# Kernel tuning notes

Hardware: AMD Instinct MI355X
Metric: run time of the kernel (lower is better)

## Reference

```python
import jax, jax.numpy as jnp
import numpy as np

BLKQ = 64
BLKK = 64
TOPK_RATIO = 0.125


def setup_inputs() -> dict:
    key = jax.random.key(0)
    ks = jax.random.split(key, 4)
    B, L, H, D = 1, 4096, 16, 64
    q = jax.random.normal(ks[0], (B, L, H, D), jnp.float32)
    k = jax.random.normal(ks[1], (B, L, H, D), jnp.float32)
    v = jax.random.normal(ks[2], (B, L, H, D), jnp.float32)
    w_proj = jax.random.normal(ks[3], (D, D), jnp.float32) * 0.02
    b_proj = jnp.zeros((D,), jnp.float32)
    return {"q": q, "k": k, "v": v, "w_proj": w_proj, "b_proj": b_proj}


def _sparse_linear_attn(q, k, v, w_proj, b_proj):
    # q,k,v: (B, L, H, D) -> (B, H, L, D)
    q = jnp.transpose(q, (0, 2, 1, 3))
    k = jnp.transpose(k, (0, 2, 1, 3))
    v = jnp.transpose(v, (0, 2, 1, 3))
    B, H, L, D = q.shape
    M, N = L // BLKQ, L // BLKK  # L chosen divisible by block sizes (no padding)
    T = max(1, int(TOPK_RATIO * N))  # selected key blocks per query block

    qb = q.reshape(B, H, M, BLKQ, D)
    kb = k.reshape(B, H, N, BLKK, D)
    vb = v.reshape(B, H, N, BLKK, D)

    # --- block map: mean-pooled block descriptors, topk key blocks per query block ---
    qm = qb.mean(axis=3)  # (B,H,M,D)
    km = kb.mean(axis=3)  # (B,H,N,D)
    blk_scores = jnp.einsum('bhmd,bhnd->bhmn', qm, km)
    _, lut = jax.lax.top_k(blk_scores, T)  # (B,H,M,T) int32

    # --- gather selected K/V blocks ---
    b_idx = jnp.arange(B)[:, None, None, None]
    h_idx = jnp.arange(H)[None, :, None, None]
    k_sel = kb[b_idx, h_idx, lut]  # (B,H,M,T,BLKK,D)
    v_sel = vb[b_idx, h_idx, lut]  # (B,H,M,T,BLKK,D)

    # --- block-sparse softmax attention over gathered keys only ---
    scale = D ** (-0.5)
    att = jnp.einsum('bhmqd,bhmtkd->bhmqtk', qb, k_sel) * scale
    att = att.reshape(B, H, M, BLKQ, T * BLKK)
    p = jax.nn.softmax(att, axis=-1)
    o_s = jnp.einsum('bhmqn,bhmnd->bhmqd', p, v_sel.reshape(B, H, M, T * BLKK, D))
    o_s = o_s.reshape(B, H, L, D)

    # --- global linear attention with softmax feature map ---
    q_fm = jax.nn.softmax(q, axis=-1)
    k_fm = jax.nn.softmax(k, axis=-1)
    kvsum = jnp.einsum('bhld,bhle->bhde', k_fm, v)  # (B,H,D,D)
    ksum = k_fm.sum(axis=2)  # (B,H,D)
    num = jnp.einsum('bhld,bhde->bhle', q_fm, kvsum)
    den = jnp.einsum('bhld,bhd->bhl', q_fm, ksum)[..., None] + 1e-6
    o_l = num / den
    o_l = jnp.einsum('bhld,ed->bhle', o_l, w_proj) + b_proj  # nn.Linear: x @ W.T + b

    o = o_s + o_l
    return jnp.transpose(o, (0, 2, 1, 3))  # (B, L, H, D)


def reference(q, k, v, w_proj, b_proj):
    return _sparse_linear_attn(q, k, v, w_proj, b_proj)
```

## Files before the change

### kernel.cpp

```cpp
#include <hip/hip_runtime.h>


#define NH   16
#define DH   64
#define NBLK 64
#define TSEL 8

typedef unsigned short u16;
typedef unsigned int   u32;
typedef __attribute__((ext_vector_type(8))) short short8;
typedef __attribute__((ext_vector_type(4))) float f4;

#define MFMA_BF16(a, b, c) __builtin_amdgcn_mfma_f32_16x16x32_bf16(a, b, c, 0, 0, 0)

__device__ __forceinline__ u16 f2bf_rne(float f) {
  u32 u = __float_as_uint(f);
  u += 0x7fffu + ((u >> 16) & 1u);
  return (u16)(u >> 16);
}
__device__ __forceinline__ u32 pk2(float a, float b) {
  return (u32)f2bf_rne(a) | ((u32)f2bf_rne(b) << 16);
}
__device__ __forceinline__ float bf2f(u16 u) { return __uint_as_float(((u32)u) << 16); }

__device__ __forceinline__ short8 frag_row(const u16* t, int row, int jblk) {
  return *(const short8*)((const char*)t + row * 128 + ((jblk ^ (row & 7)) * 16));
}

__global__ __launch_bounds__(256) void prep_kernel(const float* __restrict__ q,
                                                   const float* __restrict__ k,
                                                   const float* __restrict__ v,
                                                   u16* __restrict__ kT,
                                                   u16* __restrict__ vT,
                                                   float* __restrict__ kvsum,
                                                   float* __restrict__ ksum,
                                                   float* __restrict__ kmv,
                                                   float* __restrict__ qkp2) {
  __shared__ __align__(16) char vsl[8192];
  __shared__ __align__(16) char kfm[8192];
  __shared__ float kcol[64 * 65];
  __shared__ float redmx[256];
  __shared__ float redsm[256];
  __shared__ float kmred[256];
  __shared__ float ksred[256];
  int b = blockIdx.x;
  int n = (b >> 3) & 63;
  int h = 2 * (b & 7) + (b >> 9);
  int tid = threadIdx.x;
  int w = tid >> 6, lane = tid & 63;
  int row = lane, qd = w;
  int lq = lane & 15, quad = lane >> 4;

  float kv[16];
  {
    const float* kr = k + (size_t)(n * 64 + row) * 1024 + h * 64 + qd * 16;
#pragma unroll
    for (int c4 = 0; c4 < 4; c4++) {
      float4 a = *(const float4*)(kr + c4 * 4);
      kv[c4 * 4] = a.x; kv[c4 * 4 + 1] = a.y; kv[c4 * 4 + 2] = a.z; kv[c4 * 4 + 3] = a.w;
    }
  }
  {
    char* ktb = (char*)(kT + ((size_t)(h * 64 + n)) * 4096);
    uint4 w0 = make_uint4(pk2(kv[0], kv[1]), pk2(kv[2], kv[3]),
                          pk2(kv[4], kv[5]), pk2(kv[6], kv[7]));
    uint4 w1 = make_uint4(pk2(kv[8], kv[9]), pk2(kv[10], kv[11]),
                          pk2(kv[12], kv[13]), pk2(kv[14], kv[15]));
    *(uint4*)(ktb + row * 128 + (((2 * qd) ^ (row & 7)) * 16)) = w0;
    *(uint4*)(ktb + row * 128 + (((2 * qd + 1) ^ (row & 7)) * 16)) = w1;
  }
  {
#pragma unroll
    for (int j = 0; j < 16; j++) kcol[(qd * 16 + j) * 65 + row] = kv[j];
  }
  {
    const float* vr = v + (size_t)(n * 64 + row) * 1024 + h * 64 + qd * 16;
    int kb = row >> 3, klo = row & 7;
#pragma unroll
    for (int c4 = 0; c4 < 4; c4++) {
      float4 a = *(const float4*)(vr + c4 * 4);
      float vv[4] = {a.x, a.y, a.z, a.w};
#pragma unroll
      for (int jj = 0; jj < 4; jj++) {
        int e = qd * 16 + c4 * 4 + jj;
        *(u16*)(vsl + e * 128 + ((kb ^ (e & 7)) * 16) + klo * 2) = f2bf_rne(vv[jj]);
      }
    }
  }
  {
    float mx = kv[0];
#pragma unroll
    for (int j = 1; j < 16; j++) mx = fmaxf(mx, kv[j]);
    redmx[qd * 64 + row] = mx;
  }
  __syncthreads();
  {
    int c = tid & 63, g = tid >> 6;
    float pk = 0.f;
#pragma unroll
    for (int i = 0; i < 16; i++) pk += kcol[c * 65 + g * 16 + i];
    kmred[g * 64 + c] = pk;
  }
  {
    float mx = fmaxf(fmaxf(redmx[row], redmx[64 + row]),
                     fmaxf(redmx[128 + row], redmx[192 + row]));
    float sm = 0.f;
#pragma unroll
    for (int j = 0; j < 16; j++) { kv[j] = __expf(kv[j] - mx); sm += kv[j]; }
    redsm[qd * 64 + row] = sm;
  }
  __syncthreads();
  if (tid < 64)
    kmv[h * 4096 + n * 64 + tid] =
        (kmred[tid] + kmred[64 + tid] + kmred[128 + tid] + kmred[192 + tid]) * (1.0f / 64.0f);
  {
    float sm = redsm[row] + redsm[64 + row] + redsm[128 + row] + redsm[192 + row];
    float inv = 1.0f / sm;
    int rb = row >> 3, rlo = row & 7;
#pragma unroll
    for (int j = 0; j < 16; j++) {
      int d = qd * 16 + j;
      *(u16*)(kfm + d * 128 + (((rb) ^ (d & 7)) * 16) + rlo * 2) = f2bf_rne(kv[j] * inv);
    }
  }
  __syncthreads();

  {
    uint4* vt_out = (uint4*)(vT + ((size_t)(h * 64 + n)) * 4096);
    vt_out[tid] = ((const uint4*)vsl)[tid];
    vt_out[256 + tid] = ((const uint4*)vsl)[256 + tid];
  }
  {
    float ks = 0.f;
    short8 x0 = frag_row((const u16*)kfm, lane, 2 * w);
    short8 x1 = frag_row((const u16*)kfm, lane, 2 * w + 1);
#pragma unroll
    for (int e = 0; e < 8; e++) ks += bf2f((u16)x0[e]) + bf2f((u16)x1[e]);
    ksred[tid] = ks;
  }
  {
    f4 acc[4];
    f4 zz = {0.f, 0.f, 0.f, 0.f};
#pragma unroll
    for (int et = 0; et < 4; et++) acc[et] = zz;
#pragma unroll
    for (int ks2 = 0; ks2 < 2; ks2++) {
      short8 a_ = frag_row((const u16*)kfm, w * 16 + lq, 4 * ks2 + quad);
#pragma unroll
      for (int et = 0; et < 4; et++)
        acc[et] = MFMA_BF16(a_, frag_row((const u16*)vsl, et * 16 + lq, 4 * ks2 + quad), acc[et]);
    }
#pragma unroll
    for (int et = 0; et < 4; et++)
#pragma unroll
      for (int r = 0; r < 4; r++)
        atomicAdd(&kvsum[h * 4096 + (w * 16 + quad * 4 + r) * 64 + et * 16 + lq],
                  acc[et][r]);
  }
  __syncthreads();
  if (tid < 64)
    atomicAdd(&ksum[h * 64 + tid], ksred[tid] + ksred[64 + tid] +
                                   ksred[128 + tid] + ksred[192 + tid]);

  {
    const float* base = q + ((size_t)(n * 64 + h * 4)) * 1024 + tid * 4;
    float4 acc = {0.f, 0.f, 0.f, 0.f};
#pragma unroll
    for (int i = 0; i < 4; i++) {
      float4 a = *(const float4*)(base + (size_t)i * 1024);
      acc.x += a.x; acc.y += a.y; acc.z += a.z; acc.w += a.w;
    }
    *(float4*)(qkp2 + ((size_t)(h * 64 + n)) * 1024 + tid * 4) = acc;
  }
}

__global__ __launch_bounds__(256) void post_kernel(const float* __restrict__ qkp2,
                                                   const float* __restrict__ kmv,
                                                   const float* __restrict__ kvsum,
                                                   const float* __restrict__ wgt,
                                                   int* __restrict__ lut,
                                                   u16* __restrict__ m2t) {
  __shared__ float kv_s[64 * 65];
  __shared__ __align__(16) float wt[64 * 20];
  __shared__ __align__(16) float qr_s[4][80];
  int bx = blockIdx.x, tid = threadIdx.x;
  if (bx < 256) {
    int h = bx >> 4, w = tid >> 6, n = tid & 63;
    int m = (bx & 15) * 4 + w;
    float qsum = 0.f;
#pragma unroll
    for (int jg = 0; jg < 16; jg++)
      qsum += qkp2[((size_t)(jg * 64 + m)) * 1024 + h * 64 + n];
    qr_s[w][n] = qsum;
    __syncthreads();
    const float* kr = kmv + h * 4096 + n * 64;
    float s = 0.f;
#pragma unroll
    for (int d = 0; d < 64; d += 4) {
      float4 a = *(const float4*)(kr + d);
      float4 bb = *(const float4*)(&qr_s[w][d]);
      s += a.x * bb.x + a.y * bb.y + a.z * bb.z + a.w * bb.w;
    }
    float my = s;
    for (int t = 0; t < TSEL; t++) {
      float vv = my; int idx = n;
#pragma unroll
      for (int off = 1; off < 64; off <<= 1) {
        float ov = __shfl_xor(vv, off);
        int oi = __shfl_xor(idx, off);
        if (ov > vv || (ov == vv && oi < idx)) { vv = ov; idx = oi; }
      }
      if (n == 0) lut[(h * NBLK + m) * TSEL + t] = idx;
      if (n == idx) my = -INFINITY;
    }
  } else {
    int ib = bx - 256, h = ib >> 2, eq = ib & 3;
#pragma unroll
    for (int jj = 0; jj < 16; jj++) {
      int id2 = jj * 256 + tid;
      kv_s[(id2 >> 6) * 65 + (id2 & 63)] = kvsum[h * 4096 + id2];
    }
#pragma unroll
    for (int i = 0; i < 4; i++) {
      int f = i * 256 + tid;
      wt[(f & 63) * 20 + (f >> 6)] = wgt[(eq * 16 + (f >> 6)) * 64 + (f & 63)];
    }
    __syncthreads();
    int d = tid & 63, g = tid >> 6;
    float4 acc = {0.f, 0.f, 0.f, 0.f};
    for (int jj = 0; jj < 64; jj++) {
      float kvj = kv_s[d * 65 + jj];
      float4 wv = *(const float4*)(&wt[jj * 20 + g * 4]);
      acc.x = fmaf(kvj, wv.x, acc.x);
      acc.y = fmaf(kvj, wv.y, acc.y);
      acc.z = fmaf(kvj, wv.z, acc.z);
      acc.w = fmaf(kvj, wv.w, acc.w);
    }
    char* base = (char*)m2t + (size_t)h * 8192;
    float av[4] = {acc.x, acc.y, acc.z, acc.w};
#pragma unroll
    for (int c = 0; c < 4; c++) {
      int ee = eq * 16 + g * 4 + c;
      *(u16*)(base + ee * 128 + (((d >> 3) ^ (ee & 7)) * 16) + (d & 7) * 2) = f2bf_rne(av[c]);
    }
  }
}

__global__ __launch_bounds__(256, 5) void fused_attn_kernel(const float* __restrict__ q,
                                                            const u16* __restrict__ kT,
                                                            const u16* __restrict__ vT,
                                                            const int* __restrict__ lut,
                                                            const u16* __restrict__ m2t,
                                                            const float* __restrict__ ksum,
                                                            const float* __restrict__ bproj,
                                                            float* __restrict__ out) {
  __shared__ __align__(16) char smem[32768];
  int b = blockIdx.x;
  int m = (b >> 3) & 63;
  int h = 2 * (b & 7) + (b >> 9);
  int tid = threadIdx.x, w = tid >> 6, lane = tid & 63;
  int lq = lane & 15, quad = lane >> 4;
  u16* q_l = (u16*)smem;
  char* buf = smem + 8192;
  char* p_b = smem + 24576 + w * 2048;

  const int lb = (h * NBLK + m) * TSEL;
  int blks[8];
#pragma unroll
  for (int t = 0; t < 8; t++) blks[t] = lut[lb + t];

  {
#pragma unroll
    for (int c = 0; c < 2; c++) {
      int lo = c * 4096 + tid * 16;
      int r = lo >> 7;
      int j = ((lo >> 4) & 7) ^ (r & 7);
      const float* gp = q + ((size_t)(m * 64 + r)) * 1024 + h * 64 + j * 8;
      float4 a = *(const float4*)gp;
      float4 bb = *(const float4*)(gp + 4);
      *(uint4*)(smem + lo) = make_uint4(pk2(a.x, a.y), pk2(a.z, a.w),
                                        pk2(bb.x, bb.y), pk2(bb.z, bb.w));
    }
  }
  {
    const uint4* kt0 = (const uint4*)(kT + ((size_t)(h * 64 + blks[0])) * 4096);
    const uint4* vt0 = (const uint4*)(vT + ((size_t)(h * 64 + blks[0])) * 4096);
    ((uint4*)buf)[tid] = kt0[tid];
    ((uint4*)buf)[256 + tid] = kt0[256 + tid];
    ((uint4*)(buf + 8192))[tid] = vt0[tid];
    ((uint4*)(buf + 8192))[256 + tid] = vt0[256 + tid];
  }
  __syncthreads();

  const int qrow = w * 16 + lq;
  short8 qf[2];
#pragma unroll
  for (int ks = 0; ks < 2; ks++) qf[ks] = frag_row(q_l, qrow, 4 * ks + quad);

  float mrun = -INFINITY, lrun = 0.f;
  f4 o[4];
  f4 zz = {0.f, 0.f, 0.f, 0.f};
#pragma unroll
  for (int et = 0; et < 4; et++) o[et] = zz;

  const u16* kc = (const u16*)buf;
  const u16* vc = (const u16*)(buf + 8192);

  for (int t = 0; t < 8; t++) {
    uint4 pk0, pk1, pv0, pv1;
    if (t < 7) {
      const uint4* ktn = (const uint4*)(kT + ((size_t)(h * 64 + blks[t + 1])) * 4096);
      const uint4* vtn = (const uint4*)(vT + ((size_t)(h * 64 + blks[t + 1])) * 4096);
      pk0 = ktn[tid]; pk1 = ktn[256 + tid];
      pv0 = vtn[tid]; pv1 = vtn[256 + tid];
    }

    f4 s[4];
#pragma unroll
    for (int kt = 0; kt < 4; kt++) s[kt] = zz;
    __builtin_amdgcn_s_setprio(1);
#pragma unroll
    for (int ks = 0; ks < 2; ks++)
#pragma unroll
      for (int kt = 0; kt < 4; kt++)
        s[kt] = MFMA_BF16(frag_row(kc, kt * 16 + lq, 4 * ks + quad), qf[ks], s[kt]);
    __builtin_amdgcn_s_setprio(0);

    float mp = -INFINITY;
#pragma unroll
    for (int kt = 0; kt < 4; kt++)
#pragma unroll
      for (int r = 0; r < 4; r++) mp = fmaxf(mp, s[kt][r]);
    mp = fmaxf(mp, __shfl_xor(mp, 16));
    mp = fmaxf(mp, __shfl_xor(mp, 32));
    mp *= 0.125f;
    if (__any(mp > mrun)) {
      float mn = fmaxf(mrun, mp);
      float al = __expf(mrun - mn);
      mrun = mn;
      lrun *= al;
#pragma unroll
      for (int et = 0; et < 4; et++)
#pragma unroll
        for (int r = 0; r < 4; r++) o[et][r] *= al;
    }
    float rs_ = 0.f;
#pragma unroll
    for (int kt = 0; kt < 4; kt++) {
      float p0 = __expf(fmaf(s[kt][0], 0.125f, -mrun));
      float p1 = __expf(fmaf(s[kt][1], 0.125f, -mrun));
      float p2 = __expf(fmaf(s[kt][2], 0.125f, -mrun));
      float p3 = __expf(fmaf(s[kt][3], 0.125f, -mrun));
      rs_ += p0 + p1 + p2 + p3;
      u32 lo32 = (__float_as_uint(p0) >> 16) | (__float_as_uint(p1) & 0xffff0000u);
      u32 hi32 = (__float_as_uint(p2) >> 16) | (__float_as_uint(p3) & 0xffff0000u);
      int addr = lq * 128 + (((kt * 2 + (quad >> 1)) ^ (lq & 7)) * 16) + (quad & 1) * 8;
      *(uint2*)(p_b + addr) = make_uint2(lo32, hi32);
    }
    rs_ += __shfl_xor(rs_, 16);
    rs_ += __shfl_xor(rs_, 32);
    lrun += rs_;

    __builtin_amdgcn_s_setprio(1);
#pragma unroll
    for (int ks = 0; ks < 2; ks++) {
      short8 pf = frag_row((const u16*)p_b, lq, 4 * ks + quad);
#pragma unroll
      for (int et = 0; et < 4; et++)
        o[et] = MFMA_BF16(frag_row(vc, et * 16 + lq, 4 * ks + quad), pf, o[et]);
    }
    __builtin_amdgcn_s_setprio(0);

    if (t < 7) {
      __syncthreads();
      ((uint4*)buf)[tid] = pk0;
      ((uint4*)buf)[256 + tid] = pk1;
      ((uint4*)(buf + 8192))[tid] = pv0;
      ((uint4*)(buf + 8192))[256 + tid] = pv1;
      __syncthreads();
    }
  }

  __syncthreads();
  {
    const uint4* src = (const uint4*)((const char*)m2t + (size_t)h * 8192);
    ((uint4*)buf)[tid] = src[tid];
    ((uint4*)buf)[256 + tid] = src[256 + tid];
    if (tid < 64) {
      ((float*)(buf + 8192))[tid] = ksum[h * 64 + tid];
      ((float*)(buf + 8448))[tid] = bproj[tid];
    }
  }
  __syncthreads();
  u16* m2_l = (u16*)buf;
  float* ks_s = (float*)(buf + 8192);
  float* b_s = (float*)(buf + 8448);

  short8 qa = frag_row(q_l, qrow, 2 * quad);
  short8 qb = frag_row(q_l, qrow, 2 * quad + 1);
  float ev[16];
  float mx = -INFINITY;
#pragma unroll
  for (int j = 0; j < 8; j++) { float x = bf2f((u16)qa[j]); ev[j] = x; mx = fmaxf(mx, x); }
#pragma unroll
  for (int j = 0; j < 8; j++) { float x = bf2f((u16)qb[j]); ev[8 + j] = x; mx = fmaxf(mx, x); }
  mx = fmaxf(mx, __shfl_xor(mx, 16));
  mx = fmaxf(mx, __shfl_xor(mx, 32));
  float sum = 0.f, eks = 0.f;
#pragma unroll
  for (int j = 0; j < 16; j++) {
    float e = __expf(ev[j] - mx);
    ev[j] = e;
    sum += e;
    eks += e * ks_s[quad * 16 + j];
  }
  sum += __shfl_xor(sum, 16); sum += __shfl_xor(sum, 32);
  eks += __shfl_xor(eks, 16); eks += __shfl_xor(eks, 32);
  float invs = 1.0f / sum;
  float den = fmaf(eks, invs, 1e-6f);
  float scale = invs / den;
  uint4 e0v = make_uint4(pk2(ev[0], ev[1]), pk2(ev[2], ev[3]),
                         pk2(ev[4], ev[5]), pk2(ev[6], ev[7]));
  uint4 e1v = make_uint4(pk2(ev[8], ev[9]), pk2(ev[10], ev[11]),
                         pk2(ev[12], ev[13]), pk2(ev[14], ev[15]));
  *(uint4*)(p_b + lq * 128 + (((2 * quad) ^ (lq & 7)) * 16)) = e0v;
  *(uint4*)(p_b + lq * 128 + (((2 * quad + 1) ^ (lq & 7)) * 16)) = e1v;

  f4 oc[4];
  f4 zz2 = {0.f, 0.f, 0.f, 0.f};
#pragma unroll
  for (int et = 0; et < 4; et++) oc[et] = zz2;
  __builtin_amdgcn_s_setprio(1);
#pragma unroll
  for (int ks2 = 0; ks2 < 2; ks2++) {
    short8 ef = frag_row((const u16*)p_b, lq, 4 * ks2 + quad);
#pragma unroll
    for (int et = 0; et < 4; et++)
      oc[et] = MFMA_BF16(frag_row(m2_l, et * 16 + lq, 4 * ks2 + quad), ef, oc[et]);
  }
  __builtin_amdgcn_s_setprio(0);

  float invl = 1.0f / lrun;
  float* gp = out + ((size_t)(m * 64 + qrow)) * 1024 + h * 64 + quad * 4;
#pragma unroll
  for (int et = 0; et < 4; et++) {
    int e0 = et * 16 + quad * 4;
    float4 ov;
    ov.x = o[et][0] * invl + oc[et][0] * scale + b_s[e0 + 0];
    ov.y = o[et][1] * invl + oc[et][1] * scale + b_s[e0 + 1];
    ov.z = o[et][2] * invl + oc[et][2] * scale + b_s[e0 + 2];
    ov.w = o[et][3] * invl + oc[et][3] * scale + b_s[e0 + 3];
    *(float4*)(gp + et * 16) = ov;
  }
}

extern "C" void kernel_launch(void* const* d_in, const int* in_sizes, int n_in,
                              void* d_out, int out_size, void* d_ws, size_t ws_size,
                              hipStream_t stream) {
  const float* q = (const float*)d_in[0];
  const float* k = (const float*)d_in[1];
  const float* v = (const float*)d_in[2];
  const float* w = (const float*)d_in[3];
  const float* b = (const float*)d_in[4];
  float* out = (float*)d_out;

  u16* kT = (u16*)d_ws;
  u16* vT = kT + 4194304;
  float* qkp2 = (float*)(vT + 4194304);
  float* kmv = qkp2 + 1048576;
  int* lut = (int*)(kmv + 65536);
  float* kvsum = (float*)(lut + 8192);
  float* ksum = kvsum + 65536;
  u16* m2t = (u16*)(ksum + 1024);

  hipMemsetAsync(kvsum, 0, (65536 + 1024) * sizeof(float), stream);
  prep_kernel<<<1024, 256, 0, stream>>>(q, k, v, kT, vT, kvsum, ksum, kmv, qkp2);
  post_kernel<<<320, 256, 0, stream>>>(qkp2, kmv, kvsum, w, lut, m2t);
  fused_attn_kernel<<<1024, 256, 0, stream>>>(q, kT, vT, lut, m2t, ksum, b, out);
}
```

Baseline: 146.7 us.

## Move block top-k into attention kernel and replace atomics with partial-sum reduction

The per-query-block mean pooling and top-k block selection move from post_kernel into fused_attn_kernel, so the lut and qkp2 round trips through global memory go away. The kvsum and ksum atomics in prep_kernel become per-key-block partial writes, and post_kernel reduces them deterministically, which also removes the memset. Q fragments are now loaded directly from global memory instead of being staged through LDS. The smaller LDS footprint allows the occupancy hint to go from 5 to 6. In exchange, the partial buffer adds about 16MB of extra global writes and reads, and every attention block recomputes the block scores.

```diff
diff --git a/kernel.cpp b/kernel.cpp
--- a/kernel.cpp
+++ b/kernel.cpp
@@ -10,6 +10,7 @@
 typedef unsigned int   u32;
 typedef __attribute__((ext_vector_type(8))) short short8;
 typedef __attribute__((ext_vector_type(4))) float f4;
+typedef __attribute__((ext_vector_type(4))) u32 u32x4;
 
 #define MFMA_BF16(a, b, c) __builtin_amdgcn_mfma_f32_16x16x32_bf16(a, b, c, 0, 0, 0)
 
@@ -27,15 +28,13 @@
   return *(const short8*)((const char*)t + row * 128 + ((jblk ^ (row & 7)) * 16));
 }
 
-__global__ __launch_bounds__(256) void prep_kernel(const float* __restrict__ q,
-                                                   const float* __restrict__ k,
+__global__ __launch_bounds__(256) void prep_kernel(const float* __restrict__ k,
                                                    const float* __restrict__ v,
                                                    u16* __restrict__ kT,
                                                    u16* __restrict__ vT,
-                                                   float* __restrict__ kvsum,
-                                                   float* __restrict__ ksum,
-                                                   float* __restrict__ kmv,
-                                                   float* __restrict__ qkp2) {
+                                                   float* __restrict__ kvp,
+                                                   float* __restrict__ ksp,
+                                                   float* __restrict__ kmv) {
   __shared__ __align__(16) char vsl[8192];
   __shared__ __align__(16) char kfm[8192];
   __shared__ float kcol[64 * 65];
@@ -150,58 +149,112 @@
       for (int et = 0; et < 4; et++)
         acc[et] = MFMA_BF16(a_, frag_row((const u16*)vsl, et * 16 + lq, 4 * ks2 + quad), acc[et]);
     }
-#pragma unroll
-    for (int et = 0; et < 4; et++)
-#pragma unroll
-      for (int r = 0; r < 4; r++)
-        atomicAdd(&kvsum[h * 4096 + (w * 16 + quad * 4 + r) * 64 + et * 16 + lq],
-                  acc[et][r]);
+    float* kvb = kvp + ((size_t)(h * 64 + n)) * 4096;
+#pragma unroll
+    for (int r = 0; r < 4; r++)
+#pragma unroll
+      for (int et = 0; et < 4; et++)
+        kvb[(w * 16 + quad * 4 + r) * 64 + et * 16 + lq] = acc[et][r];
   }
   __syncthreads();
   if (tid < 64)
-    atomicAdd(&ksum[h * 64 + tid], ksred[tid] + ksred[64 + tid] +
-                                   ksred[128 + tid] + ksred[192 + tid]);
-
-  {
-    const float* base = q + ((size_t)(n * 64 + h * 4)) * 1024 + tid * 4;
-    float4 acc = {0.f, 0.f, 0.f, 0.f};
-#pragma unroll
-    for (int i = 0; i < 4; i++) {
-      float4 a = *(const float4*)(base + (size_t)i * 1024);
-      acc.x += a.x; acc.y += a.y; acc.z += a.z; acc.w += a.w;
-    }
-    *(float4*)(qkp2 + ((size_t)(h * 64 + n)) * 1024 + tid * 4) = acc;
-  }
-}
-
-__global__ __launch_bounds__(256) void post_kernel(const float* __restrict__ qkp2,
-                                                   const float* __restrict__ kmv,
-                                                   const float* __restrict__ kvsum,
+    ksp[((size_t)(h * 64 + n)) * 64 + tid] = ksred[tid] + ksred[64 + tid] +
+                                             ksred[128 + tid] + ksred[192 + tid];
+}
+
+__global__ __launch_bounds__(256) void post_kernel(const float* __restrict__ kvp,
+                                                   const float* __restrict__ ksp,
                                                    const float* __restrict__ wgt,
-                                                   int* __restrict__ lut,
-                                                   u16* __restrict__ m2t) {
-  __shared__ float kv_s[64 * 65];
-  __shared__ __align__(16) float wt[64 * 20];
-  __shared__ __align__(16) float qr_s[4][80];
+                                                   u16* __restrict__ m2t,
+                                                   float* __restrict__ ksum) {
+  __shared__ float kr[4][64];
+  __shared__ float wl[64 * 65];
   int bx = blockIdx.x, tid = threadIdx.x;
-  if (bx < 256) {
-    int h = bx >> 4, w = tid >> 6, n = tid & 63;
-    int m = (bx & 15) * 4 + w;
-    float qsum = 0.f;
-#pragma unroll
-    for (int jg = 0; jg < 16; jg++)
-      qsum += qkp2[((size_t)(jg * 64 + m)) * 1024 + h * 64 + n];
-    qr_s[w][n] = qsum;
-    __syncthreads();
-    const float* kr = kmv + h * 4096 + n * 64;
+  int h = bx >> 4, dq = bx & 15;
+  int j = tid & 63, rr = tid >> 6;
+
+  {
+    size_t off = (size_t)(dq * 4 + rr) * 64 + j;
+    const float* base = kvp + (size_t)h * 64 * 4096 + off;
+    float s0 = 0.f, s1 = 0.f, s2 = 0.f, s3 = 0.f;
+#pragma unroll
+    for (int n4 = 0; n4 < 16; n4++) {
+      s0 += base[(size_t)(n4 * 4 + 0) * 4096];
+      s1 += base[(size_t)(n4 * 4 + 1) * 4096];
+      s2 += base[(size_t)(n4 * 4 + 2) * 4096];
+      s3 += base[(size_t)(n4 * 4 + 3) * 4096];
+    }
+    kr[rr][j] = (s0 + s1) + (s2 + s3);
+  }
+#pragma unroll
+  for (int i = 0; i < 16; i++) {
+    int f = i * 256 + tid;
+    wl[(f >> 6) * 65 + (f & 63)] = wgt[f];
+  }
+  __syncthreads();
+
+  {
+    int e = tid & 63, rr2 = tid >> 6;
+    float acc = 0.f;
+#pragma unroll
+    for (int jj = 0; jj < 64; jj++) acc = fmaf(kr[rr2][jj], wl[e * 65 + jj], acc);
+    int d = dq * 4 + rr2;
+    *(u16*)((char*)m2t + (size_t)h * 8192 + e * 128 +
+            (((d >> 3) ^ (e & 7)) * 16) + (d & 7) * 2) = f2bf_rne(acc);
+  }
+  if (dq == 0 && tid < 64) {
+    const float* base = ksp + (size_t)h * 64 * 64 + tid;
     float s = 0.f;
 #pragma unroll
-    for (int d = 0; d < 64; d += 4) {
-      float4 a = *(const float4*)(kr + d);
-      float4 bb = *(const float4*)(&qr_s[w][d]);
-      s += a.x * bb.x + a.y * bb.y + a.z * bb.z + a.w * bb.w;
-    }
+    for (int n = 0; n < 64; n++) s += base[(size_t)n * 64];
+    ksum[h * 64 + tid] = s;
+  }
+}
+
+__global__ __launch_bounds__(256, 6) void fused_attn_kernel(const float* __restrict__ q,
+                                                            const u16* __restrict__ kT,
+                                                            const u16* __restrict__ vT,
+                                                            const float* __restrict__ kmv,
+                                                            const u16* __restrict__ m2t,
+                                                            const float* __restrict__ ksum,
+                                                            const float* __restrict__ bproj,
+                                                            float* __restrict__ out) {
+  __shared__ __align__(16) char smem[24576];
+  int b = blockIdx.x;
+  int m = (b >> 3) & 63;
+  int h = 2 * (b & 7) + (b >> 9);
+  int tid = threadIdx.x, w = tid >> 6, lane = tid & 63;
+  int lq = lane & 15, quad = lane >> 4;
+  char* buf = smem;
+  char* p_b = smem + 16384 + w * 2048;
+  float* km_s = (float*)smem;
+  float* qmp = (float*)(smem + 20480);
+  float* qmf = (float*)(smem + 21504);
+
+  {
+    int c = tid & 63, g = tid >> 6;
+    const float* qcol = q + ((size_t)(m * 64 + g * 16)) * 1024 + h * 64 + c;
+    float qp = 0.f;
+#pragma unroll
+    for (int i = 0; i < 16; i++) qp += qcol[(size_t)i * 1024];
+    qmp[g * 64 + c] = qp;
+#pragma unroll
+    for (int i = 0; i < 16; i++) {
+      int idx = i * 256 + tid;
+      km_s[(idx >> 6) * 65 + (idx & 63)] = kmv[h * 4096 + idx];
+    }
+  }
+  __syncthreads();
+  if (tid < 64) qmf[tid] = qmp[tid] + qmp[64 + tid] + qmp[128 + tid] + qmp[192 + tid];
+  __syncthreads();
+  int blks[8];
+  {
+    int n = lane;
+    float s = 0.f;
+#pragma unroll
+    for (int d = 0; d < 64; d++) s += qmf[d] * km_s[n * 65 + d];
     float my = s;
+#pragma unroll
     for (int t = 0; t < TSEL; t++) {
       float vv = my; int idx = n;
 #pragma unroll
@@ -210,78 +263,25 @@
         int oi = __shfl_xor(idx, off);
         if (ov > vv || (ov == vv && oi < idx)) { vv = ov; idx = oi; }
       }
-      if (n == 0) lut[(h * NBLK + m) * TSEL + t] = idx;
-      if (n == idx) my = -INFINITY;
-    }
-  } else {
-    int ib = bx - 256, h = ib >> 2, eq = ib & 3;
-#pragma unroll
-    for (int jj = 0; jj < 16; jj++) {
-      int id2 = jj * 256 + tid;
-      kv_s[(id2 >> 6) * 65 + (id2 & 63)] = kvsum[h * 4096 + id2];
-    }
-#pragma unroll
-    for (int i = 0; i < 4; i++) {
-      int f = i * 256 + tid;
-      wt[(f & 63) * 20 + (f >> 6)] = wgt[(eq * 16 + (f >> 6)) * 64 + (f & 63)];
-    }
-    __syncthreads();
-    int d = tid & 63, g = tid >> 6;
-    float4 acc = {0.f, 0.f, 0.f, 0.f};
-    for (int jj = 0; jj < 64; jj++) {
-      float kvj = kv_s[d * 65 + jj];
-      float4 wv = *(const float4*)(&wt[jj * 20 + g * 4]);
-      acc.x = fmaf(kvj, wv.x, acc.x);
-      acc.y = fmaf(kvj, wv.y, acc.y);
-      acc.z = fmaf(kvj, wv.z, acc.z);
-      acc.w = fmaf(kvj, wv.w, acc.w);
-    }
-    char* base = (char*)m2t + (size_t)h * 8192;
-    float av[4] = {acc.x, acc.y, acc.z, acc.w};
-#pragma unroll
-    for (int c = 0; c < 4; c++) {
-      int ee = eq * 16 + g * 4 + c;
-      *(u16*)(base + ee * 128 + (((d >> 3) ^ (ee & 7)) * 16) + (d & 7) * 2) = f2bf_rne(av[c]);
-    }
-  }
-}
-
-__global__ __launch_bounds__(256, 5) void fused_attn_kernel(const float* __restrict__ q,
-                                                            const u16* __restrict__ kT,
-                                                            const u16* __restrict__ vT,
-                                                            const int* __restrict__ lut,
-                                                            const u16* __restrict__ m2t,
-                                                            const float* __restrict__ ksum,
-                                                            const float* __restrict__ bproj,
-                                                            float* __restrict__ out) {
-  __shared__ __align__(16) char smem[32768];
-  int b = blockIdx.x;
-  int m = (b >> 3) & 63;
-  int h = 2 * (b & 7) + (b >> 9);
-  int tid = threadIdx.x, w = tid >> 6, lane = tid & 63;
-  int lq = lane & 15, quad = lane >> 4;
-  u16* q_l = (u16*)smem;
-  char* buf = smem + 8192;
-  char* p_b = smem + 24576 + w * 2048;
-
-  const int lb = (h * NBLK + m) * TSEL;
-  int blks[8];
-#pragma unroll
-  for (int t = 0; t < 8; t++) blks[t] = lut[lb + t];
-
-  {
-#pragma unroll
-    for (int c = 0; c < 2; c++) {
-      int lo = c * 4096 + tid * 16;
-      int r = lo >> 7;
-      int j = ((lo >> 4) & 7) ^ (r & 7);
-      const float* gp = q + ((size_t)(m * 64 + r)) * 1024 + h * 64 + j * 8;
-      float4 a = *(const float4*)gp;
-      float4 bb = *(const float4*)(gp + 4);
-      *(uint4*)(smem + lo) = make_uint4(pk2(a.x, a.y), pk2(a.z, a.w),
-                                        pk2(bb.x, bb.y), pk2(bb.z, bb.w));
-    }
-  }
+      int sel = __builtin_amdgcn_readfirstlane(idx);
+      blks[t] = sel;
+      if (n == sel) my = -INFINITY;
+    }
+  }
+  __syncthreads();
+
+  const int qrow = w * 16 + lq;
+  const float* qr_g = q + ((size_t)(m * 64 + qrow)) * 1024 + h * 64;
+  short8 qf[2];
+#pragma unroll
+  for (int ks = 0; ks < 2; ks++) {
+    const float* gp = qr_g + (4 * ks + quad) * 8;
+    float4 a = *(const float4*)gp;
+    float4 bb = *(const float4*)(gp + 4);
+    u32x4 tt = {pk2(a.x, a.y), pk2(a.z, a.w), pk2(bb.x, bb.y), pk2(bb.z, bb.w)};
+    qf[ks] = __builtin_bit_cast(short8, tt);
+  }
+
   {
     const uint4* kt0 = (const uint4*)(kT + ((size_t)(h * 64 + blks[0])) * 4096);
     const uint4* vt0 = (const uint4*)(vT + ((size_t)(h * 64 + blks[0])) * 4096);
@@ -291,11 +291,6 @@
     ((uint4*)(buf + 8192))[256 + tid] = vt0[256 + tid];
   }
   __syncthreads();
-
-  const int qrow = w * 16 + lq;
-  short8 qf[2];
-#pragma unroll
-  for (int ks = 0; ks < 2; ks++) qf[ks] = frag_row(q_l, qrow, 4 * ks + quad);
 
   float mrun = -INFINITY, lrun = 0.f;
   f4 o[4];
@@ -396,14 +391,14 @@
   float* ks_s = (float*)(buf + 8192);
   float* b_s = (float*)(buf + 8448);
 
-  short8 qa = frag_row(q_l, qrow, 2 * quad);
-  short8 qb = frag_row(q_l, qrow, 2 * quad + 1);
   float ev[16];
   float mx = -INFINITY;
 #pragma unroll
-  for (int j = 0; j < 8; j++) { float x = bf2f((u16)qa[j]); ev[j] = x; mx = fmaxf(mx, x); }
-#pragma unroll
-  for (int j = 0; j < 8; j++) { float x = bf2f((u16)qb[j]); ev[8 + j] = x; mx = fmaxf(mx, x); }
+  for (int c4 = 0; c4 < 4; c4++) {
+    float4 a = *(const float4*)(qr_g + quad * 16 + c4 * 4);
+    ev[c4 * 4] = a.x; ev[c4 * 4 + 1] = a.y; ev[c4 * 4 + 2] = a.z; ev[c4 * 4 + 3] = a.w;
+    mx = fmaxf(mx, fmaxf(fmaxf(a.x, a.y), fmaxf(a.z, a.w)));
+  }
   mx = fmaxf(mx, __shfl_xor(mx, 16));
   mx = fmaxf(mx, __shfl_xor(mx, 32));
   float sum = 0.f, eks = 0.f;
@@ -466,15 +461,13 @@
 
   u16* kT = (u16*)d_ws;
   u16* vT = kT + 4194304;
-  float* qkp2 = (float*)(vT + 4194304);
-  float* kmv = qkp2 + 1048576;
-  int* lut = (int*)(kmv + 65536);
-  float* kvsum = (float*)(lut + 8192);
-  float* ksum = kvsum + 65536;
+  float* kvp = (float*)(vT + 4194304);
+  float* ksp = kvp + 4194304;
+  float* kmv = ksp + 65536;
+  float* ksum = kmv + 65536;
   u16* m2t = (u16*)(ksum + 1024);
 
-  hipMemsetAsync(kvsum, 0, (65536 + 1024) * sizeof(float), stream);
-  prep_kernel<<<1024, 256, 0, stream>>>(q, k, v, kT, vT, kvsum, ksum, kmv, qkp2);
-  post_kernel<<<320, 256, 0, stream>>>(qkp2, kmv, kvsum, w, lut, m2t);
-  fused_attn_kernel<<<1024, 256, 0, stream>>>(q, kT, vT, lut, m2t, ksum, b, out);
-}
+  prep_kernel<<<1024, 256, 0, stream>>>(k, v, kT, vT, kvp, ksp, kmv);
+  post_kernel<<<256, 256, 0, stream>>>(kvp, ksp, w, m2t, ksum);
+  fused_attn_kernel<<<1024, 256, 0, stream>>>(q, kT, vT, kmv, m2t, ksum, b, out);
+}
```

Result: faster. 137.0 us (-6.6%).
